# Optimization experiments

Hardware: AMD Instinct MI355X
Metric: run time of the kernel (lower is better)

Reference implementation:

```python
import jax, jax.numpy as jnp
import numpy as np

D_MODEL = 1024
HEAD_DIM = D_MODEL // 16  # num_heads=16, used only for the softmax scale
EPS = 1e-5


def _layernorm(x, g, b):
    mu = jnp.mean(x, axis=-1, keepdims=True)
    var = jnp.var(x, axis=-1, keepdims=True)
    return (x - mu) * jax.lax.rsqrt(var + EPS) * g + b


def setup_inputs() -> dict:
    key = jax.random.key(0)
    ks = jax.random.split(key, 16)
    d, dff = D_MODEL, 4 * D_MODEL
    s = 1.0 / np.sqrt(d)
    inp = {
        "x": jax.random.normal(ks[0], (4, 2048, d), dtype=jnp.float32),
        "wq": jax.random.normal(ks[1], (d, d), dtype=jnp.float32) * s,
        "bq": jnp.zeros((d,), jnp.float32),
        "wk": jax.random.normal(ks[2], (d, d), dtype=jnp.float32) * s,
        "bk": jnp.zeros((d,), jnp.float32),
        "wv": jax.random.normal(ks[3], (d, d), dtype=jnp.float32) * s,
        "bv": jnp.zeros((d,), jnp.float32),
        "wo": jax.random.normal(ks[4], (d, d), dtype=jnp.float32) * s,
        "bo": jnp.zeros((d,), jnp.float32),
        "w1": jax.random.normal(ks[5], (d, dff), dtype=jnp.float32) * s,
        "b1": jnp.zeros((dff,), jnp.float32),
        "w2": jax.random.normal(ks[6], (dff, d), dtype=jnp.float32) * (1.0 / np.sqrt(dff)),
        "b2": jnp.zeros((d,), jnp.float32),
        "g1": jnp.ones((d,), jnp.float32),
        "be1": jnp.zeros((d,), jnp.float32),
        "g2": jnp.ones((d,), jnp.float32),
        "be2": jnp.zeros((d,), jnp.float32),
    }
    return inp


def reference(x, wq, bq, wk, bk, wv, bv, wo, bo, w1, b1, w2, b2, g1, be1, g2, be2):
    # --- attention sub-block (NOTE: no head split in original module) ---
    residual = x
    h = _layernorm(x, g1, be1)
    q = h @ wq + bq
    k = h @ wk + bk
    v = h @ wv + bv
    scale = 1.0 / np.sqrt(HEAD_DIM)
    scores = jnp.einsum("bsd,btd->bst", q, k) * scale  # [B,S,S]
    attn = jax.nn.softmax(scores, axis=-1)
    ctx = jnp.einsum("bst,btd->bsd", attn, v)
    x = ctx @ wo + bo + residual
    # --- MLP sub-block ---
    residual = x
    h = _layernorm(x, g2, be2)
    h = jax.nn.gelu(h @ w1 + b1, approximate=False)
    return h @ w2 + b2 + residual
```

## Files before the change

kernel.cpp:

```cpp
#include <hip/hip_runtime.h>
#include <hip/hip_bf16.h>

typedef __hip_bfloat16 bf16;
typedef __attribute__((ext_vector_type(8))) short short8;
typedef __attribute__((ext_vector_type(4))) float floatx4;
typedef __attribute__((address_space(3))) char c3;

template <int V> struct ic { static constexpr int value = V; };

__device__ __forceinline__ unsigned short f2bf(float x) {
  unsigned u = __builtin_bit_cast(unsigned, x);
  unsigned r = (u + 0x7fffu + ((u >> 16) & 1u)) >> 16;
  return (unsigned short)r;
}

#define GLL(g, l) __builtin_amdgcn_global_load_lds(                                  \
    (const __attribute__((address_space(1))) void*)(g),                              \
    (__attribute__((address_space(3))) void*)(l), 16, 0, 0)

template <int N> __device__ __forceinline__ void vmwait() {
  asm volatile("s_waitcnt vmcnt(%0)" ::"i"(N) : "memory");
}
template <int OFF> __device__ __forceinline__ short8 dsr(unsigned a) {
  short8 r;
  asm volatile("ds_read_b128 %0, %1 offset:%2" : "=v"(r) : "v"(a), "i"(OFF));
  return r;
}
__device__ __forceinline__ void lgkm0_fence() {
  asm volatile("s_waitcnt lgkmcnt(0)" ::: "memory");
  __builtin_amdgcn_sched_barrier(0);
}

__global__ __launch_bounds__(256) void wtrans_kernel(const float* __restrict__ in,
                                                     bf16* __restrict__ out,
                                                     int K, int N) {
  __shared__ float tile[32][33];
  int tx = threadIdx.x, ty = threadIdx.y;
  int n0 = blockIdx.x * 32, k0 = blockIdx.y * 32;
#pragma unroll
  for (int i = 0; i < 32; i += 8)
    tile[ty + i][tx] = in[(size_t)(k0 + ty + i) * N + (n0 + tx)];
  __syncthreads();
#pragma unroll
  for (int i = 0; i < 32; i += 8)
    out[(size_t)(n0 + ty + i) * K + (k0 + tx)] = __float2bfloat16(tile[tx][ty + i]);
}

__global__ __launch_bounds__(256) void ln_kernel(const float* __restrict__ x,
                                                 const float* __restrict__ g,
                                                 const float* __restrict__ b,
                                                 bf16* __restrict__ out) {
  const int D = 1024;
  size_t row = blockIdx.x;
  int t = threadIdx.x;
  float4 v = ((const float4*)(x + row * D))[t];
  float s  = v.x + v.y + v.z + v.w;
  float ss = v.x * v.x + v.y * v.y + v.z * v.z + v.w * v.w;
#pragma unroll
  for (int off = 32; off > 0; off >>= 1) {
    s  += __shfl_xor(s, off);
    ss += __shfl_xor(ss, off);
  }
  __shared__ float rs[4], rss[4];
  int wv = t >> 6;
  if ((t & 63) == 0) { rs[wv] = s; rss[wv] = ss; }
  __syncthreads();
  s  = rs[0] + rs[1] + rs[2] + rs[3];
  ss = rss[0] + rss[1] + rss[2] + rss[3];
  float mu  = s * (1.f / D);
  float inv = rsqrtf(ss * (1.f / D) - mu * mu + 1e-5f);
  float4 gv = ((const float4*)g)[t];
  float4 bv = ((const float4*)b)[t];
  ushort4 o;
  o.x = f2bf((v.x - mu) * inv * gv.x + bv.x);
  o.y = f2bf((v.y - mu) * inv * gv.y + bv.y);
  o.z = f2bf((v.z - mu) * inv * gv.z + bv.z);
  o.w = f2bf((v.w - mu) * inv * gv.w + bv.w);
  ((ushort4*)(out + row * D))[t] = o;
}

__global__ __launch_bounds__(256) void softmax_kernel(float* sc) {
  const int S = 2048;
  float* p = sc + (size_t)blockIdx.x * S;
  int t = threadIdx.x;
  float4 v0 = ((const float4*)p)[2 * t];
  float4 v1 = ((const float4*)p)[2 * t + 1];
  float f[8] = {v0.x, v0.y, v0.z, v0.w, v1.x, v1.y, v1.z, v1.w};
  float m = f[0];
#pragma unroll
  for (int j = 1; j < 8; ++j) m = fmaxf(m, f[j]);
#pragma unroll
  for (int off = 32; off > 0; off >>= 1) m = fmaxf(m, __shfl_xor(m, off));
  __shared__ float r1[4], r2[4];
  int wv = t >> 6;
  if ((t & 63) == 0) r1[wv] = m;
  __syncthreads();
  m = fmaxf(fmaxf(r1[0], r1[1]), fmaxf(r1[2], r1[3]));
  float s = 0.f;
#pragma unroll
  for (int j = 0; j < 8; ++j) { f[j] = __expf(f[j] - m); s += f[j]; }
#pragma unroll
  for (int off = 32; off > 0; off >>= 1) s += __shfl_xor(s, off);
  if ((t & 63) == 0) r2[wv] = s;
  __syncthreads();
  s = r2[0] + r2[1] + r2[2] + r2[3];
  float inv = 1.f / s;
  unsigned u0 = f2bf(f[0] * inv), u1 = f2bf(f[1] * inv);
  unsigned u2 = f2bf(f[2] * inv), u3 = f2bf(f[3] * inv);
  unsigned u4 = f2bf(f[4] * inv), u5 = f2bf(f[5] * inv);
  unsigned u6 = f2bf(f[6] * inv), u7 = f2bf(f[7] * inv);
  uint4 o;
  o.x = u0 | (u1 << 16);
  o.y = u2 | (u3 << 16);
  o.z = u4 | (u5 << 16);
  o.w = u6 | (u7 << 16);
  ((uint4*)p)[t] = o;
}

template <int NF, bool OUT_BF16, bool HAS_BIAS, bool HAS_RES, bool GELU, bool VTR>
__global__ __launch_bounds__(512, 2) void gemm7(
    const bf16* __restrict__ A, int lda, size_t sA,
    const bf16* __restrict__ BT, int ldb, size_t sB,
    void* Cv, size_t sC,
    const float* __restrict__ bias, const float* res, bf16* vtr,
    int N, int K, float alpha, int gx, int gy) {
  constexpr int BN = NF * 64;
  constexpr int NI = NF / 2;
  constexpr int BHALF = NF == 4 ? 16384 : 8192;
  __shared__ __align__(16) char lds_storage[65536 + (NF == 4 ? 65536 : 32768)];
  const unsigned ldsAu = (unsigned)(uintptr_t)(c3*)lds_storage;
  const unsigned ldsBu = ldsAu + 65536;

  const int tid = threadIdx.x;
  const int lane = tid & 63;
  const int wave = tid >> 6;
  const int wm = wave >> 2, wn = wave & 3;
  const int lr = lane & 15, lq = lane >> 4;

  int id = blockIdx.x;
  const int nwg = gridDim.x;
  if ((nwg & 7) == 0) id = (id & 7) * (nwg >> 3) + (id >> 3);
  const int bx = id % gx;
  const int rem = id / gx;
  const int by = rem % gy;
  const int bz = rem / gy;
  const int m0 = by * 256, n0 = bx * BN;

  const int srow = tid >> 3;
  const int schunk = ((tid & 7) ^ (srow & 7)) * 8;
  const bf16* gA = A + sA * bz + (size_t)(m0 + srow) * lda + schunk;
  const bf16* gB = BT + sB * bz + (size_t)(n0 + srow) * ldb + schunk;

  const int nk = K >> 6;

  auto stA = [&](int tt, int h) {
    const bf16* s = gA + (size_t)(h * 128) * lda + (size_t)tt * 64;
    char* d = lds_storage + (((tt & 1) * 2 + h) << 14) + tid * 16;
    GLL(s, d);
    GLL(s + (size_t)64 * lda, d + 8192);
  };
  auto stB = [&](int tt, int h) {
    const bf16* s = gB + (size_t)(h * (BN / 2)) * ldb + (size_t)tt * 64;
    char* d = lds_storage + 65536 + ((tt & 1) * 2 + h) * BHALF + tid * 16;
    GLL(s, d);
    if constexpr (NF == 4) GLL(s + (size_t)64 * ldb, d + 8192);
  };

  const unsigned aB0 = (wm * 64 + lr) * 128 + ((lq ^ (lr & 7)) << 4);
  const unsigned bRow = (NF == 4) ? (wn * 32 + lr) : (wn * 16 + lr);
  const unsigned bB0 = bRow * 128 + ((lq ^ (lr & 7)) << 4);

  floatx4 acc[2][2][4][NI] = {};

  stA(0, 0); stB(0, 0); stB(0, 1); stA(0, 1);
  stA(1, 0); stB(1, 0); stB(1, 1);
  vmwait<NF == 4 ? 10 : 7>();
  __builtin_amdgcn_s_barrier();

  auto tile_body = [&](int t, auto modeC) {
    constexpr int MODE = decltype(modeC)::value;
    constexpr int W0  = MODE < 2 ? (NF == 4 ? 10 : 8) : 2;
    constexpr int W1  = MODE == 0 ? (NF == 4 ? 12 : 9)
                                  : (MODE == 1 ? (NF == 4 ? 8 : 6) : 0);
    constexpr int W23 = MODE == 0 ? (NF == 4 ? 10 : 7)
                                  : (MODE == 1 ? (NF == 4 ? 4 : 3) : -1);
    const unsigned As0 = ldsAu + (((t & 1) * 2 + 0) << 14);
    const unsigned As1 = As0 + 16384;
    const unsigned Bs0 = ldsBu + ((t & 1) * 2 + 0) * BHALF;
    const unsigned Bs1 = Bs0 + BHALF;
    short8 a0[4], a1[4], b0[NI], b1[NI], bb0[NI], bb1[NI];

    {
      const unsigned aA = As0 + aB0, aX = aA ^ 64;
      a0[0] = dsr<0>(aA);  a0[1] = dsr<2048>(aA);  a0[2] = dsr<4096>(aA);  a0[3] = dsr<6144>(aA);
      a1[0] = dsr<0>(aX);  a1[1] = dsr<2048>(aX);  a1[2] = dsr<4096>(aX);  a1[3] = dsr<6144>(aX);
      const unsigned bA = Bs0 + bB0, bX = bA ^ 64;
      bb0[0] = dsr<0>(bA); bb1[0] = dsr<0>(bX);
      if constexpr (NI > 1) { bb0[1] = dsr<2048>(bA); bb1[1] = dsr<2048>(bX); }
    }
    if constexpr (MODE < 2) stA(t + 1, 1);
    lgkm0_fence();
    __builtin_amdgcn_s_setprio(1);
#pragma unroll
    for (int mi = 0; mi < 4; ++mi)
#pragma unroll
      for (int ni = 0; ni < NI; ++ni)
        acc[0][0][mi][ni] = __builtin_amdgcn_mfma_f32_16x16x32_bf16(a0[mi], bb0[ni], acc[0][0][mi][ni], 0, 0, 0);
#pragma unroll
    for (int mi = 0; mi < 4; ++mi)
#pragma unroll
      for (int ni = 0; ni < NI; ++ni)
        acc[0][0][mi][ni] = __builtin_amdgcn_mfma_f32_16x16x32_bf16(a1[mi], bb1[ni], acc[0][0][mi][ni], 0, 0, 0);
    __builtin_amdgcn_s_setprio(0);
    vmwait<W0>();
    __builtin_amdgcn_s_barrier();

    {
      const unsigned bA = Bs1 + bB0, bX = bA ^ 64;
      b0[0] = dsr<0>(bA); b1[0] = dsr<0>(bX);
      if constexpr (NI > 1) { b0[1] = dsr<2048>(bA); b1[1] = dsr<2048>(bX); }
    }
    if constexpr (MODE == 0) { stA(t + 2, 0); stB(t + 2, 0); }
    lgkm0_fence();
    __builtin_amdgcn_s_setprio(1);
#pragma unroll
    for (int mi = 0; mi < 4; ++mi)
#pragma unroll
      for (int ni = 0; ni < NI; ++ni)
        acc[0][1][mi][ni] = __builtin_amdgcn_mfma_f32_16x16x32_bf16(a0[mi], b0[ni], acc[0][1][mi][ni], 0, 0, 0);
#pragma unroll
    for (int mi = 0; mi < 4; ++mi)
#pragma unroll
      for (int ni = 0; ni < NI; ++ni)
        acc[0][1][mi][ni] = __builtin_amdgcn_mfma_f32_16x16x32_bf16(a1[mi], b1[ni], acc[0][1][mi][ni], 0, 0, 0);
    __builtin_amdgcn_s_setprio(0);
    vmwait<W1>();
    __builtin_amdgcn_s_barrier();

    {
      const unsigned aA = As1 + aB0, aX = aA ^ 64;
      a0[0] = dsr<0>(aA);  a0[1] = dsr<2048>(aA);  a0[2] = dsr<4096>(aA);  a0[3] = dsr<6144>(aA);
      a1[0] = dsr<0>(aX);  a1[1] = dsr<2048>(aX);  a1[2] = dsr<4096>(aX);  a1[3] = dsr<6144>(aX);
    }
    if constexpr (MODE == 0) stB(t + 2, 1);
    lgkm0_fence();
    __builtin_amdgcn_s_setprio(1);
#pragma unroll
    for (int mi = 0; mi < 4; ++mi)
#pragma unroll
      for (int ni = 0; ni < NI; ++ni)
        acc[1][1][mi][ni] = __builtin_amdgcn_mfma_f32_16x16x32_bf16(a0[mi], b0[ni], acc[1][1][mi][ni], 0, 0, 0);
#pragma unroll
    for (int mi = 0; mi < 4; ++mi)
#pragma unroll
      for (int ni = 0; ni < NI; ++ni)
        acc[1][1][mi][ni] = __builtin_amdgcn_mfma_f32_16x16x32_bf16(a1[mi], b1[ni], acc[1][1][mi][ni], 0, 0, 0);
#pragma unroll
    for (int mi = 0; mi < 4; ++mi)
#pragma unroll
      for (int ni = 0; ni < NI; ++ni)
        acc[1][0][mi][ni] = __builtin_amdgcn_mfma_f32_16x16x32_bf16(a0[mi], bb0[ni], acc[1][0][mi][ni], 0, 0, 0);
#pragma unroll
    for (int mi = 0; mi < 4; ++mi)
#pragma unroll
      for (int ni = 0; ni < NI; ++ni)
        acc[1][0][mi][ni] = __builtin_amdgcn_mfma_f32_16x16x32_bf16(a1[mi], bb1[ni], acc[1][0][mi][ni], 0, 0, 0);
    __builtin_amdgcn_s_setprio(0);
    if constexpr (W23 >= 0) {
      vmwait<W23>();
      __builtin_amdgcn_s_barrier();
    }
  };

  for (int t = 0; t + 2 < nk; ++t) tile_body(t, ic<0>{});
  tile_body(nk - 2, ic<1>{});
  tile_body(nk - 1, ic<2>{});

  float* Cf = (float*)Cv;
  bf16* Cb = (bf16*)Cv;
  const size_t cb = sC * bz;
#pragma unroll
  for (int mq = 0; mq < 2; ++mq)
#pragma unroll
    for (int nq = 0; nq < 2; ++nq)
#pragma unroll
      for (int mi = 0; mi < 4; ++mi) {
        const int row = m0 + mq * 128 + wm * 64 + mi * 16 + lq * 4;
#pragma unroll
        for (int ni = 0; ni < NI; ++ni) {
          const int col = n0 + nq * (BN / 2) + wn * (BN / 8) + ni * 16 + lr;
          const float bb = HAS_BIAS ? bias[col] : 0.f;
#pragma unroll
          for (int r = 0; r < 4; ++r) {
            float val = acc[mq][nq][mi][ni][r] * alpha + bb;
            if (GELU) val = 0.5f * val * (1.f + erff(val * 0.70710678118654752f));
            if (HAS_RES) val += res[(size_t)(row + r) * N + col];
            const size_t idx = cb + (size_t)(row + r) * N + col;
            if (OUT_BF16) Cb[idx] = __float2bfloat16(val);
            else Cf[idx] = val;
            if (VTR) {
              if (col >= 2048) {
                const int rr = row + r;
                vtr[(((size_t)(rr >> 11) << 10) + (col - 2048)) * 2048 + (rr & 2047)] =
                    __float2bfloat16(val);
              }
            }
          }
        }
      }
}

extern "C" void kernel_launch(void* const* d_in, const int* in_sizes, int n_in,
                              void* d_out, int out_size, void* d_ws, size_t ws_size,
                              hipStream_t stream) {
  const int B = 4, S = 2048, D = 1024, DFF = 4096;
  const int M = B * S;
  const float* x   = (const float*)d_in[0];
  const float* wq  = (const float*)d_in[1];
  const float* bq  = (const float*)d_in[2];
  const float* wk  = (const float*)d_in[3];
  const float* bk  = (const float*)d_in[4];
  const float* wv  = (const float*)d_in[5];
  const float* bv  = (const float*)d_in[6];
  const float* wo  = (const float*)d_in[7];
  const float* bo  = (const float*)d_in[8];
  const float* w1  = (const float*)d_in[9];
  const float* b1  = (const float*)d_in[10];
  const float* w2  = (const float*)d_in[11];
  const float* b2  = (const float*)d_in[12];
  const float* g1  = (const float*)d_in[13];
  const float* be1 = (const float*)d_in[14];
  const float* g2  = (const float*)d_in[15];
  const float* be2 = (const float*)d_in[16];
  float* out = (float*)d_out;

  char* wsb = (char*)d_ws;
  const size_t MB1 = 1ull << 20;
  bf16* wqkvT = (bf16*)(wsb + 0 * MB1);
  bf16* woT   = (bf16*)(wsb + 6 * MB1);
  bf16* w1T   = (bf16*)(wsb + 8 * MB1);
  bf16* w2T   = (bf16*)(wsb + 16 * MB1);
  float* bqkv = (float*)(wsb + 24 * MB1);
  bf16* h     = (bf16*)(wsb + 25 * MB1);
  bf16* qkv   = (bf16*)(wsb + 41 * MB1);
  bf16* hidden = (bf16*)(wsb + 41 * MB1);
  bf16* vTall = (bf16*)(wsb + 89 * MB1);
  float* sc   = (float*)(wsb + 105 * MB1);

  int chunk = 1;
  if (ws_size > 105 * MB1) {
    size_t c = (ws_size - 105 * MB1) / (16 * MB1);
    chunk = (int)(c > 4 ? 4 : (c < 1 ? 1 : c));
  }

  dim3 tb(32, 8);
  wtrans_kernel<<<dim3(32, 32), tb, 0, stream>>>(wq, wqkvT, D, D);
  wtrans_kernel<<<dim3(32, 32), tb, 0, stream>>>(wk, wqkvT + (size_t)1024 * 1024, D, D);
  wtrans_kernel<<<dim3(32, 32), tb, 0, stream>>>(wv, wqkvT + (size_t)2048 * 1024, D, D);
  wtrans_kernel<<<dim3(32, 32), tb, 0, stream>>>(wo, woT, D, D);
  wtrans_kernel<<<dim3(128, 32), tb, 0, stream>>>(w1, w1T, D, DFF);
  wtrans_kernel<<<dim3(32, 128), tb, 0, stream>>>(w2, w2T, DFF, D);
  hipMemcpyAsync(bqkv, bq, 4096, hipMemcpyDeviceToDevice, stream);
  hipMemcpyAsync(bqkv + 1024, bk, 4096, hipMemcpyDeviceToDevice, stream);
  hipMemcpyAsync(bqkv + 2048, bv, 4096, hipMemcpyDeviceToDevice, stream);

  ln_kernel<<<M, 256, 0, stream>>>(x, g1, be1, h);

  gemm7<2, true, true, false, false, true><<<24 * 32, 512, 0, stream>>>(
      h, D, 0, wqkvT, D, 0, qkv, 0, bqkv, nullptr, vTall, 3072, D, 1.f, 24, 32);

  for (int b0 = 0; b0 < B; b0 += chunk) {
    int c = (B - b0 < chunk) ? (B - b0) : chunk;
    gemm7<4, false, false, false, false, false><<<64 * c, 512, 0, stream>>>(
        qkv + (size_t)b0 * S * 3072, 3072, (size_t)S * 3072,
        qkv + (size_t)b0 * S * 3072 + 1024, 3072, (size_t)S * 3072,
        sc, (size_t)S * S, nullptr, nullptr, nullptr, S, D, 0.125f, 8, 8);
    softmax_kernel<<<c * S, 256, 0, stream>>>(sc);
    gemm7<2, true, false, false, false, false><<<64 * c, 512, 0, stream>>>(
        (const bf16*)sc, 2 * S, (size_t)S * 2 * S,
        vTall + (size_t)b0 * D * S, S, (size_t)D * S,
        h + (size_t)b0 * S * D, (size_t)S * D, nullptr, nullptr, nullptr, D, S, 1.f, 8, 8);
  }

  gemm7<2, false, true, true, false, false><<<8 * 32, 512, 0, stream>>>(
      h, D, 0, woT, D, 0, out, 0, bo, x, nullptr, D, D, 1.f, 8, 32);

  ln_kernel<<<M, 256, 0, stream>>>(out, g2, be2, h);

  gemm7<4, true, true, false, true, false><<<16 * 32, 512, 0, stream>>>(
      h, D, 0, w1T, D, 0, hidden, 0, b1, nullptr, nullptr, DFF, D, 1.f, 16, 32);

  gemm7<2, false, true, true, false, false><<<8 * 32, 512, 0, stream>>>(
      hidden, DFF, 0, w2T, DFF, 0, out, 0, b2, out, nullptr, D, DFF, 1.f, 8, 32);
}
```

Baseline: 459.2 us.

## Rewrite GEMM main loop with cross-tile register prefetch and drop 256-wide tile variant

```diff
diff --git a/kernel.cpp b/kernel.cpp
--- a/kernel.cpp
+++ b/kernel.cpp
@@ -21,15 +21,16 @@
 template <int N> __device__ __forceinline__ void vmwait() {
   asm volatile("s_waitcnt vmcnt(%0)" ::"i"(N) : "memory");
 }
+template <int N> __device__ __forceinline__ void lgkwait() {
+  asm volatile("s_waitcnt lgkmcnt(%0)" ::"i"(N) : "memory");
+  __builtin_amdgcn_sched_barrier(0);
+}
 template <int OFF> __device__ __forceinline__ short8 dsr(unsigned a) {
   short8 r;
   asm volatile("ds_read_b128 %0, %1 offset:%2" : "=v"(r) : "v"(a), "i"(OFF));
   return r;
 }
-__device__ __forceinline__ void lgkm0_fence() {
-  asm volatile("s_waitcnt lgkmcnt(0)" ::: "memory");
-  __builtin_amdgcn_sched_barrier(0);
-}
+#define MFMA_(d, a, b) d = __builtin_amdgcn_mfma_f32_16x16x32_bf16(a, b, d, 0, 0, 0)
 
 __global__ __launch_bounds__(256) void wtrans_kernel(const float* __restrict__ in,
                                                      bf16* __restrict__ out,
@@ -117,17 +118,14 @@
   ((uint4*)p)[t] = o;
 }
 
-template <int NF, bool OUT_BF16, bool HAS_BIAS, bool HAS_RES, bool GELU, bool VTR>
-__global__ __launch_bounds__(512, 2) void gemm7(
+template <bool OUT_BF16, bool HAS_BIAS, bool HAS_RES, bool GELU, bool VTR>
+__global__ __launch_bounds__(512, 2) void gemm8(
     const bf16* __restrict__ A, int lda, size_t sA,
     const bf16* __restrict__ BT, int ldb, size_t sB,
     void* Cv, size_t sC,
     const float* __restrict__ bias, const float* res, bf16* vtr,
     int N, int K, float alpha, int gx, int gy) {
-  constexpr int BN = NF * 64;
-  constexpr int NI = NF / 2;
-  constexpr int BHALF = NF == 4 ? 16384 : 8192;
-  __shared__ __align__(16) char lds_storage[65536 + (NF == 4 ? 65536 : 32768)];
+  __shared__ __align__(16) char lds_storage[65536 + 32768];
   const unsigned ldsAu = (unsigned)(uintptr_t)(c3*)lds_storage;
   const unsigned ldsBu = ldsAu + 65536;
 
@@ -144,7 +142,7 @@
   const int rem = id / gx;
   const int by = rem % gy;
   const int bz = rem / gy;
-  const int m0 = by * 256, n0 = bx * BN;
+  const int m0 = by * 256, n0 = bx * 128;
 
   const int srow = tid >> 3;
   const int schunk = ((tid & 7) ^ (srow & 7)) * 8;
@@ -160,121 +158,102 @@
     GLL(s + (size_t)64 * lda, d + 8192);
   };
   auto stB = [&](int tt, int h) {
-    const bf16* s = gB + (size_t)(h * (BN / 2)) * ldb + (size_t)tt * 64;
-    char* d = lds_storage + 65536 + ((tt & 1) * 2 + h) * BHALF + tid * 16;
+    const bf16* s = gB + (size_t)(h * 64) * ldb + (size_t)tt * 64;
+    char* d = lds_storage + 65536 + ((tt & 1) * 2 + h) * 8192 + tid * 16;
     GLL(s, d);
-    if constexpr (NF == 4) GLL(s + (size_t)64 * ldb, d + 8192);
   };
 
   const unsigned aB0 = (wm * 64 + lr) * 128 + ((lq ^ (lr & 7)) << 4);
-  const unsigned bRow = (NF == 4) ? (wn * 32 + lr) : (wn * 16 + lr);
-  const unsigned bB0 = bRow * 128 + ((lq ^ (lr & 7)) << 4);
-
-  floatx4 acc[2][2][4][NI] = {};
+  const unsigned bB0 = (wn * 16 + lr) * 128 + ((lq ^ (lr & 7)) << 4);
+
+  floatx4 acc[2][2][4] = {};
+  short8 am0k0[4], am0k1[4];
+  short8 bn0Ak0, bn0Ak1, bn0Bk0, bn0Bk1;
 
   stA(0, 0); stB(0, 0); stB(0, 1); stA(0, 1);
-  stA(1, 0); stB(1, 0); stB(1, 1);
-  vmwait<NF == 4 ? 10 : 7>();
+  stA(1, 0); stB(1, 0); stB(1, 1); stA(1, 1);
+  vmwait<8>();
   __builtin_amdgcn_s_barrier();
-
-  auto tile_body = [&](int t, auto modeC) {
+  {
+    const unsigned aA = ldsAu + aB0, aX = aA ^ 64;
+    am0k0[0] = dsr<0>(aA); am0k0[1] = dsr<2048>(aA); am0k0[2] = dsr<4096>(aA); am0k0[3] = dsr<6144>(aA);
+    am0k1[0] = dsr<0>(aX); am0k1[1] = dsr<2048>(aX); am0k1[2] = dsr<4096>(aX); am0k1[3] = dsr<6144>(aX);
+    const unsigned bA = ldsBu + bB0;
+    bn0Ak0 = dsr<0>(bA); bn0Ak1 = dsr<0>(bA ^ 64);
+  }
+
+  auto body = [&](int t, auto modeC, short8& bu0, short8& bu1, short8& bw0, short8& bw1) {
     constexpr int MODE = decltype(modeC)::value;
-    constexpr int W0  = MODE < 2 ? (NF == 4 ? 10 : 8) : 2;
-    constexpr int W1  = MODE == 0 ? (NF == 4 ? 12 : 9)
-                                  : (MODE == 1 ? (NF == 4 ? 8 : 6) : 0);
-    constexpr int W23 = MODE == 0 ? (NF == 4 ? 10 : 7)
-                                  : (MODE == 1 ? (NF == 4 ? 4 : 3) : -1);
-    const unsigned As0 = ldsAu + (((t & 1) * 2 + 0) << 14);
-    const unsigned As1 = As0 + 16384;
-    const unsigned Bs0 = ldsBu + ((t & 1) * 2 + 0) * BHALF;
-    const unsigned Bs1 = Bs0 + BHALF;
-    short8 a0[4], a1[4], b0[NI], b1[NI], bb0[NI], bb1[NI];
-
+    const unsigned As1 = ldsAu + ((((unsigned)t & 1) * 2 + 1) << 14);
+    const unsigned Bs1 = ldsBu + (((unsigned)t & 1) * 2 + 1) * 8192;
+
+    short8 bn1k0, bn1k1;
     {
-      const unsigned aA = As0 + aB0, aX = aA ^ 64;
-      a0[0] = dsr<0>(aA);  a0[1] = dsr<2048>(aA);  a0[2] = dsr<4096>(aA);  a0[3] = dsr<6144>(aA);
-      a1[0] = dsr<0>(aX);  a1[1] = dsr<2048>(aX);  a1[2] = dsr<4096>(aX);  a1[3] = dsr<6144>(aX);
-      const unsigned bA = Bs0 + bB0, bX = bA ^ 64;
-      bb0[0] = dsr<0>(bA); bb1[0] = dsr<0>(bX);
-      if constexpr (NI > 1) { bb0[1] = dsr<2048>(bA); bb1[1] = dsr<2048>(bX); }
+      const unsigned bA = Bs1 + bB0;
+      bn1k0 = dsr<0>(bA); bn1k1 = dsr<0>(bA ^ 64);
     }
-    if constexpr (MODE < 2) stA(t + 1, 1);
-    lgkm0_fence();
+    lgkwait<2>();
     __builtin_amdgcn_s_setprio(1);
 #pragma unroll
-    for (int mi = 0; mi < 4; ++mi)
-#pragma unroll
-      for (int ni = 0; ni < NI; ++ni)
-        acc[0][0][mi][ni] = __builtin_amdgcn_mfma_f32_16x16x32_bf16(a0[mi], bb0[ni], acc[0][0][mi][ni], 0, 0, 0);
-#pragma unroll
-    for (int mi = 0; mi < 4; ++mi)
-#pragma unroll
-      for (int ni = 0; ni < NI; ++ni)
-        acc[0][0][mi][ni] = __builtin_amdgcn_mfma_f32_16x16x32_bf16(a1[mi], bb1[ni], acc[0][0][mi][ni], 0, 0, 0);
+    for (int mi = 0; mi < 4; ++mi) MFMA_(acc[0][0][mi], am0k0[mi], bu0);
+#pragma unroll
+    for (int mi = 0; mi < 4; ++mi) MFMA_(acc[0][0][mi], am0k1[mi], bu1);
     __builtin_amdgcn_s_setprio(0);
-    vmwait<W0>();
+    vmwait<MODE == 2 ? 0 : 6>();
     __builtin_amdgcn_s_barrier();
 
+    short8 am1k0[4], am1k1[4];
     {
-      const unsigned bA = Bs1 + bB0, bX = bA ^ 64;
-      b0[0] = dsr<0>(bA); b1[0] = dsr<0>(bX);
-      if constexpr (NI > 1) { b0[1] = dsr<2048>(bA); b1[1] = dsr<2048>(bX); }
+      const unsigned aA = As1 + aB0, aX = aA ^ 64;
+      am1k0[0] = dsr<0>(aA); am1k0[1] = dsr<2048>(aA); am1k0[2] = dsr<4096>(aA); am1k0[3] = dsr<6144>(aA);
+      am1k1[0] = dsr<0>(aX); am1k1[1] = dsr<2048>(aX); am1k1[2] = dsr<4096>(aX); am1k1[3] = dsr<6144>(aX);
     }
     if constexpr (MODE == 0) { stA(t + 2, 0); stB(t + 2, 0); }
-    lgkm0_fence();
+    lgkwait<8>();
     __builtin_amdgcn_s_setprio(1);
 #pragma unroll
-    for (int mi = 0; mi < 4; ++mi)
-#pragma unroll
-      for (int ni = 0; ni < NI; ++ni)
-        acc[0][1][mi][ni] = __builtin_amdgcn_mfma_f32_16x16x32_bf16(a0[mi], b0[ni], acc[0][1][mi][ni], 0, 0, 0);
-#pragma unroll
-    for (int mi = 0; mi < 4; ++mi)
-#pragma unroll
-      for (int ni = 0; ni < NI; ++ni)
-        acc[0][1][mi][ni] = __builtin_amdgcn_mfma_f32_16x16x32_bf16(a1[mi], b1[ni], acc[0][1][mi][ni], 0, 0, 0);
+    for (int mi = 0; mi < 4; ++mi) MFMA_(acc[0][1][mi], am0k0[mi], bn1k0);
+#pragma unroll
+    for (int mi = 0; mi < 4; ++mi) MFMA_(acc[0][1][mi], am0k1[mi], bn1k1);
     __builtin_amdgcn_s_setprio(0);
-    vmwait<W1>();
-    __builtin_amdgcn_s_barrier();
-
-    {
-      const unsigned aA = As1 + aB0, aX = aA ^ 64;
-      a0[0] = dsr<0>(aA);  a0[1] = dsr<2048>(aA);  a0[2] = dsr<4096>(aA);  a0[3] = dsr<6144>(aA);
-      a1[0] = dsr<0>(aX);  a1[1] = dsr<2048>(aX);  a1[2] = dsr<4096>(aX);  a1[3] = dsr<6144>(aX);
+    if constexpr (MODE == 0) { vmwait<6>(); __builtin_amdgcn_s_barrier(); }
+    else if constexpr (MODE == 1) { vmwait<3>(); __builtin_amdgcn_s_barrier(); }
+
+    if constexpr (MODE < 2) {
+      const unsigned aA = ldsAu + ((((unsigned)(t + 1) & 1) * 2) << 14) + aB0, aX = aA ^ 64;
+      am0k0[0] = dsr<0>(aA); am0k0[1] = dsr<2048>(aA); am0k0[2] = dsr<4096>(aA); am0k0[3] = dsr<6144>(aA);
+      am0k1[0] = dsr<0>(aX); am0k1[1] = dsr<2048>(aX); am0k1[2] = dsr<4096>(aX); am0k1[3] = dsr<6144>(aX);
+      const unsigned bA = ldsBu + (((unsigned)(t + 1) & 1) * 2) * 8192 + bB0;
+      bw0 = dsr<0>(bA); bw1 = dsr<0>(bA ^ 64);
     }
     if constexpr (MODE == 0) stB(t + 2, 1);
-    lgkm0_fence();
+    if constexpr (MODE < 2) lgkwait<10>();
+    else lgkwait<0>();
     __builtin_amdgcn_s_setprio(1);
 #pragma unroll
-    for (int mi = 0; mi < 4; ++mi)
-#pragma unroll
-      for (int ni = 0; ni < NI; ++ni)
-        acc[1][1][mi][ni] = __builtin_amdgcn_mfma_f32_16x16x32_bf16(a0[mi], b0[ni], acc[1][1][mi][ni], 0, 0, 0);
-#pragma unroll
-    for (int mi = 0; mi < 4; ++mi)
-#pragma unroll
-      for (int ni = 0; ni < NI; ++ni)
-        acc[1][1][mi][ni] = __builtin_amdgcn_mfma_f32_16x16x32_bf16(a1[mi], b1[ni], acc[1][1][mi][ni], 0, 0, 0);
-#pragma unroll
-    for (int mi = 0; mi < 4; ++mi)
-#pragma unroll
-      for (int ni = 0; ni < NI; ++ni)
-        acc[1][0][mi][ni] = __builtin_amdgcn_mfma_f32_16x16x32_bf16(a0[mi], bb0[ni], acc[1][0][mi][ni], 0, 0, 0);
-#pragma unroll
-    for (int mi = 0; mi < 4; ++mi)
-#pragma unroll
-      for (int ni = 0; ni < NI; ++ni)
-        acc[1][0][mi][ni] = __builtin_amdgcn_mfma_f32_16x16x32_bf16(a1[mi], bb1[ni], acc[1][0][mi][ni], 0, 0, 0);
+    for (int mi = 0; mi < 4; ++mi) MFMA_(acc[1][1][mi], am1k0[mi], bn1k0);
+#pragma unroll
+    for (int mi = 0; mi < 4; ++mi) MFMA_(acc[1][1][mi], am1k1[mi], bn1k1);
     __builtin_amdgcn_s_setprio(0);
-    if constexpr (W23 >= 0) {
-      vmwait<W23>();
-      __builtin_amdgcn_s_barrier();
-    }
+    if constexpr (MODE < 2) __builtin_amdgcn_s_barrier();
+
+    if constexpr (MODE == 0) stA(t + 2, 1);
+    __builtin_amdgcn_s_setprio(1);
+#pragma unroll
+    for (int mi = 0; mi < 4; ++mi) MFMA_(acc[1][0][mi], am1k0[mi], bu0);
+#pragma unroll
+    for (int mi = 0; mi < 4; ++mi) MFMA_(acc[1][0][mi], am1k1[mi], bu1);
+    __builtin_amdgcn_s_setprio(0);
+    if constexpr (MODE == 0) { vmwait<8>(); __builtin_amdgcn_s_barrier(); }
+    else if constexpr (MODE == 1) { vmwait<2>(); __builtin_amdgcn_s_barrier(); }
   };
 
-  for (int t = 0; t + 2 < nk; ++t) tile_body(t, ic<0>{});
-  tile_body(nk - 2, ic<1>{});
-  tile_body(nk - 1, ic<2>{});
+  for (int t = 0; t + 2 < nk; t += 2) {
+    body(t, ic<0>{}, bn0Ak0, bn0Ak1, bn0Bk0, bn0Bk1);
+    body(t + 1, ic<0>{}, bn0Bk0, bn0Bk1, bn0Ak0, bn0Ak1);
+  }
+  body(nk - 2, ic<1>{}, bn0Ak0, bn0Ak1, bn0Bk0, bn0Bk1);
+  body(nk - 1, ic<2>{}, bn0Bk0, bn0Bk1, bn0Ak0, bn0Ak1);
 
   float* Cf = (float*)Cv;
   bf16* Cb = (bf16*)Cv;
@@ -286,24 +265,21 @@
 #pragma unroll
       for (int mi = 0; mi < 4; ++mi) {
         const int row = m0 + mq * 128 + wm * 64 + mi * 16 + lq * 4;
-#pragma unroll
-        for (int ni = 0; ni < NI; ++ni) {
-          const int col = n0 + nq * (BN / 2) + wn * (BN / 8) + ni * 16 + lr;
-          const float bb = HAS_BIAS ? bias[col] : 0.f;
-#pragma unroll
-          for (int r = 0; r < 4; ++r) {
-            float val = acc[mq][nq][mi][ni][r] * alpha + bb;
-            if (GELU) val = 0.5f * val * (1.f + erff(val * 0.70710678118654752f));
-            if (HAS_RES) val += res[(size_t)(row + r) * N + col];
-            const size_t idx = cb + (size_t)(row + r) * N + col;
-            if (OUT_BF16) Cb[idx] = __float2bfloat16(val);
-            else Cf[idx] = val;
-            if (VTR) {
-              if (col >= 2048) {
-                const int rr = row + r;
-                vtr[(((size_t)(rr >> 11) << 10) + (col - 2048)) * 2048 + (rr & 2047)] =
-                    __float2bfloat16(val);
-              }
+        const int col = n0 + nq * 64 + wn * 16 + lr;
+        const float bb = HAS_BIAS ? bias[col] : 0.f;
+#pragma unroll
+        for (int r = 0; r < 4; ++r) {
+          float val = acc[mq][nq][mi][r] * alpha + bb;
+          if (GELU) val = 0.5f * val * (1.f + erff(val * 0.70710678118654752f));
+          if (HAS_RES) val += res[(size_t)(row + r) * N + col];
+          const size_t idx = cb + (size_t)(row + r) * N + col;
+          if (OUT_BF16) Cb[idx] = __float2bfloat16(val);
+          else Cf[idx] = val;
+          if (VTR) {
+            if (col >= 2048) {
+              const int rr = row + r;
+              vtr[(((size_t)(rr >> 11) << 10) + (col - 2048)) * 2048 + (rr & 2047)] =
+                  __float2bfloat16(val);
             }
           }
         }
@@ -366,30 +342,30 @@
 
   ln_kernel<<<M, 256, 0, stream>>>(x, g1, be1, h);
 
-  gemm7<2, true, true, false, false, true><<<24 * 32, 512, 0, stream>>>(
+  gemm8<true, true, false, false, true><<<24 * 32, 512, 0, stream>>>(
       h, D, 0, wqkvT, D, 0, qkv, 0, bqkv, nullptr, vTall, 3072, D, 1.f, 24, 32);
 
   for (int b0 = 0; b0 < B; b0 += chunk) {
     int c = (B - b0 < chunk) ? (B - b0) : chunk;
-    gemm7<4, false, false, false, false, false><<<64 * c, 512, 0, stream>>>(
+    gemm8<false, false, false, false, false><<<128 * c, 512, 0, stream>>>(
         qkv + (size_t)b0 * S * 3072, 3072, (size_t)S * 3072,
         qkv + (size_t)b0 * S * 3072 + 1024, 3072, (size_t)S * 3072,
-        sc, (size_t)S * S, nullptr, nullptr, nullptr, S, D, 0.125f, 8, 8);
+        sc, (size_t)S * S, nullptr, nullptr, nullptr, S, D, 0.125f, 16, 8);
     softmax_kernel<<<c * S, 256, 0, stream>>>(sc);
-    gemm7<2, true, false, false, false, false><<<64 * c, 512, 0, stream>>>(
+    gemm8<true, false, false, false, false><<<64 * c, 512, 0, stream>>>(
         (const bf16*)sc, 2 * S, (size_t)S * 2 * S,
         vTall + (size_t)b0 * D * S, S, (size_t)D * S,
         h + (size_t)b0 * S * D, (size_t)S * D, nullptr, nullptr, nullptr, D, S, 1.f, 8, 8);
   }
 
-  gemm7<2, false, true, true, false, false><<<8 * 32, 512, 0, stream>>>(
+  gemm8<false, true, true, false, false><<<8 * 32, 512, 0, stream>>>(
       h, D, 0, woT, D, 0, out, 0, bo, x, nullptr, D, D, 1.f, 8, 32);
 
   ln_kernel<<<M, 256, 0, stream>>>(out, g2, be2, h);
 
-  gemm7<4, true, true, false, true, false><<<16 * 32, 512, 0, stream>>>(
-      h, D, 0, w1T, D, 0, hidden, 0, b1, nullptr, nullptr, DFF, D, 1.f, 16, 32);
-
-  gemm7<2, false, true, true, false, false><<<8 * 32, 512, 0, stream>>>(
+  gemm8<true, true, false, true, false><<<32 * 32, 512, 0, stream>>>(
+      h, D, 0, w1T, D, 0, hidden, 0, b1, nullptr, nullptr, DFF, D, 1.f, 32, 32);
+
+  gemm8<false, true, true, false, false><<<8 * 32, 512, 0, stream>>>(
       hidden, DFF, 0, w2T, DFF, 0, out, 0, b2, out, nullptr, D, DFF, 1.f, 8, 32);
 }
```

New measurement: 463.9 us. Within noise of the previous version (+1.0%).

## Merge weight transposes into one launch and run softmax one wave per row

Applied to the files above, without the earlier changes.

```diff
diff --git a/kernel.cpp b/kernel.cpp
--- a/kernel.cpp
+++ b/kernel.cpp
@@ -31,12 +31,46 @@
   __builtin_amdgcn_sched_barrier(0);
 }
 
-__global__ __launch_bounds__(256) void wtrans_kernel(const float* __restrict__ in,
-                                                     bf16* __restrict__ out,
-                                                     int K, int N) {
+__global__ __launch_bounds__(256) void wtrans_all(
+    const float* __restrict__ wq, const float* __restrict__ wk,
+    const float* __restrict__ wv, const float* __restrict__ wo,
+    const float* __restrict__ w1, const float* __restrict__ w2,
+    bf16* __restrict__ wqkvT, bf16* __restrict__ woT,
+    bf16* __restrict__ w1T, bf16* __restrict__ w2T,
+    const float* __restrict__ bq, const float* __restrict__ bk,
+    const float* __restrict__ bv, float* __restrict__ bqkv) {
+  const int id = blockIdx.x;
+  if (id == 12288) {
+    int t = threadIdx.y * 32 + threadIdx.x;
+    for (int i = t; i < 1024; i += 256) {
+      bqkv[i] = bq[i];
+      bqkv[1024 + i] = bk[i];
+      bqkv[2048 + i] = bv[i];
+    }
+    return;
+  }
+  const float* in;
+  bf16* out;
+  int K, N, bx, by;
+  if (id < 4096) {
+    const int seg = id >> 10, r = id & 1023;
+    bx = r & 31; by = r >> 5; K = 1024; N = 1024;
+    if (seg == 0) { in = wq; out = wqkvT; }
+    else if (seg == 1) { in = wk; out = wqkvT + (size_t)1024 * 1024; }
+    else if (seg == 2) { in = wv; out = wqkvT + (size_t)2048 * 1024; }
+    else { in = wo; out = woT; }
+  } else if (id < 8192) {
+    const int r = id - 4096;
+    bx = r & 127; by = r >> 7; K = 1024; N = 4096;
+    in = w1; out = w1T;
+  } else {
+    const int r = id - 8192;
+    bx = r & 31; by = r >> 5; K = 4096; N = 1024;
+    in = w2; out = w2T;
+  }
   __shared__ float tile[32][33];
-  int tx = threadIdx.x, ty = threadIdx.y;
-  int n0 = blockIdx.x * 32, k0 = blockIdx.y * 32;
+  const int tx = threadIdx.x, ty = threadIdx.y;
+  const int n0 = bx * 32, k0 = by * 32;
 #pragma unroll
   for (int i = 0; i < 32; i += 8)
     tile[ty + i][tx] = in[(size_t)(k0 + ty + i) * N + (n0 + tx)];
@@ -79,42 +113,35 @@
   ((ushort4*)(out + row * D))[t] = o;
 }
 
-__global__ __launch_bounds__(256) void softmax_kernel(float* sc) {
+__global__ __launch_bounds__(256) void softmax_wave(float* sc) {
   const int S = 2048;
-  float* p = sc + (size_t)blockIdx.x * S;
-  int t = threadIdx.x;
-  float4 v0 = ((const float4*)p)[2 * t];
-  float4 v1 = ((const float4*)p)[2 * t + 1];
-  float f[8] = {v0.x, v0.y, v0.z, v0.w, v1.x, v1.y, v1.z, v1.w};
+  const int wave = threadIdx.x >> 6, lane = threadIdx.x & 63;
+  float* p = sc + ((size_t)blockIdx.x * 4 + wave) * S;
+  float f[32];
+  const float4* pv = (const float4*)p;
+#pragma unroll
+  for (int j = 0; j < 8; ++j) {
+    float4 v = pv[lane + 64 * j];
+    f[4 * j] = v.x; f[4 * j + 1] = v.y; f[4 * j + 2] = v.z; f[4 * j + 3] = v.w;
+  }
   float m = f[0];
 #pragma unroll
-  for (int j = 1; j < 8; ++j) m = fmaxf(m, f[j]);
+  for (int j = 1; j < 32; ++j) m = fmaxf(m, f[j]);
 #pragma unroll
   for (int off = 32; off > 0; off >>= 1) m = fmaxf(m, __shfl_xor(m, off));
-  __shared__ float r1[4], r2[4];
-  int wv = t >> 6;
-  if ((t & 63) == 0) r1[wv] = m;
-  __syncthreads();
-  m = fmaxf(fmaxf(r1[0], r1[1]), fmaxf(r1[2], r1[3]));
   float s = 0.f;
 #pragma unroll
-  for (int j = 0; j < 8; ++j) { f[j] = __expf(f[j] - m); s += f[j]; }
+  for (int j = 0; j < 32; ++j) { f[j] = __expf(f[j] - m); s += f[j]; }
 #pragma unroll
   for (int off = 32; off > 0; off >>= 1) s += __shfl_xor(s, off);
-  if ((t & 63) == 0) r2[wv] = s;
-  __syncthreads();
-  s = r2[0] + r2[1] + r2[2] + r2[3];
-  float inv = 1.f / s;
-  unsigned u0 = f2bf(f[0] * inv), u1 = f2bf(f[1] * inv);
-  unsigned u2 = f2bf(f[2] * inv), u3 = f2bf(f[3] * inv);
-  unsigned u4 = f2bf(f[4] * inv), u5 = f2bf(f[5] * inv);
-  unsigned u6 = f2bf(f[6] * inv), u7 = f2bf(f[7] * inv);
-  uint4 o;
-  o.x = u0 | (u1 << 16);
-  o.y = u2 | (u3 << 16);
-  o.z = u4 | (u5 << 16);
-  o.w = u6 | (u7 << 16);
-  ((uint4*)p)[t] = o;
+  const float inv = 1.f / s;
+  uint2* po = (uint2*)p;
+#pragma unroll
+  for (int j = 0; j < 8; ++j) {
+    unsigned lo = (unsigned)f2bf(f[4 * j] * inv) | ((unsigned)f2bf(f[4 * j + 1] * inv) << 16);
+    unsigned hi = (unsigned)f2bf(f[4 * j + 2] * inv) | ((unsigned)f2bf(f[4 * j + 3] * inv) << 16);
+    po[lane + 64 * j] = make_uint2(lo, hi);
+  }
 }
 
 template <int NF, bool OUT_BF16, bool HAS_BIAS, bool HAS_RES, bool GELU, bool VTR>
@@ -215,10 +242,11 @@
     vmwait<W0>();
     __builtin_amdgcn_s_barrier();
 
+    short8 b0l[NI], b1l[NI];
     {
       const unsigned bA = Bs1 + bB0, bX = bA ^ 64;
-      b0[0] = dsr<0>(bA); b1[0] = dsr<0>(bX);
-      if constexpr (NI > 1) { b0[1] = dsr<2048>(bA); b1[1] = dsr<2048>(bX); }
+      b0l[0] = dsr<0>(bA); b1l[0] = dsr<0>(bX);
+      if constexpr (NI > 1) { b0l[1] = dsr<2048>(bA); b1l[1] = dsr<2048>(bX); }
     }
     if constexpr (MODE == 0) { stA(t + 2, 0); stB(t + 2, 0); }
     lgkm0_fence();
@@ -227,12 +255,12 @@
     for (int mi = 0; mi < 4; ++mi)
 #pragma unroll
       for (int ni = 0; ni < NI; ++ni)
-        acc[0][1][mi][ni] = __builtin_amdgcn_mfma_f32_16x16x32_bf16(a0[mi], b0[ni], acc[0][1][mi][ni], 0, 0, 0);
-#pragma unroll
-    for (int mi = 0; mi < 4; ++mi)
-#pragma unroll
-      for (int ni = 0; ni < NI; ++ni)
-        acc[0][1][mi][ni] = __builtin_amdgcn_mfma_f32_16x16x32_bf16(a1[mi], b1[ni], acc[0][1][mi][ni], 0, 0, 0);
+        acc[0][1][mi][ni] = __builtin_amdgcn_mfma_f32_16x16x32_bf16(a0[mi], b0l[ni], acc[0][1][mi][ni], 0, 0, 0);
+#pragma unroll
+    for (int mi = 0; mi < 4; ++mi)
+#pragma unroll
+      for (int ni = 0; ni < NI; ++ni)
+        acc[0][1][mi][ni] = __builtin_amdgcn_mfma_f32_16x16x32_bf16(a1[mi], b1l[ni], acc[0][1][mi][ni], 0, 0, 0);
     __builtin_amdgcn_s_setprio(0);
     vmwait<W1>();
     __builtin_amdgcn_s_barrier();
@@ -249,12 +277,12 @@
     for (int mi = 0; mi < 4; ++mi)
 #pragma unroll
       for (int ni = 0; ni < NI; ++ni)
-        acc[1][1][mi][ni] = __builtin_amdgcn_mfma_f32_16x16x32_bf16(a0[mi], b0[ni], acc[1][1][mi][ni], 0, 0, 0);
-#pragma unroll
-    for (int mi = 0; mi < 4; ++mi)
-#pragma unroll
-      for (int ni = 0; ni < NI; ++ni)
-        acc[1][1][mi][ni] = __builtin_amdgcn_mfma_f32_16x16x32_bf16(a1[mi], b1[ni], acc[1][1][mi][ni], 0, 0, 0);
+        acc[1][1][mi][ni] = __builtin_amdgcn_mfma_f32_16x16x32_bf16(a0[mi], b0l[ni], acc[1][1][mi][ni], 0, 0, 0);
+#pragma unroll
+    for (int mi = 0; mi < 4; ++mi)
+#pragma unroll
+      for (int ni = 0; ni < NI; ++ni)
+        acc[1][1][mi][ni] = __builtin_amdgcn_mfma_f32_16x16x32_bf16(a1[mi], b1l[ni], acc[1][1][mi][ni], 0, 0, 0);
 #pragma unroll
     for (int mi = 0; mi < 4; ++mi)
 #pragma unroll
@@ -353,16 +381,8 @@
     chunk = (int)(c > 4 ? 4 : (c < 1 ? 1 : c));
   }
 
-  dim3 tb(32, 8);
-  wtrans_kernel<<<dim3(32, 32), tb, 0, stream>>>(wq, wqkvT, D, D);
-  wtrans_kernel<<<dim3(32, 32), tb, 0, stream>>>(wk, wqkvT + (size_t)1024 * 1024, D, D);
-  wtrans_kernel<<<dim3(32, 32), tb, 0, stream>>>(wv, wqkvT + (size_t)2048 * 1024, D, D);
-  wtrans_kernel<<<dim3(32, 32), tb, 0, stream>>>(wo, woT, D, D);
-  wtrans_kernel<<<dim3(128, 32), tb, 0, stream>>>(w1, w1T, D, DFF);
-  wtrans_kernel<<<dim3(32, 128), tb, 0, stream>>>(w2, w2T, DFF, D);
-  hipMemcpyAsync(bqkv, bq, 4096, hipMemcpyDeviceToDevice, stream);
-  hipMemcpyAsync(bqkv + 1024, bk, 4096, hipMemcpyDeviceToDevice, stream);
-  hipMemcpyAsync(bqkv + 2048, bv, 4096, hipMemcpyDeviceToDevice, stream);
+  wtrans_all<<<12289, dim3(32, 8), 0, stream>>>(
+      wq, wk, wv, wo, w1, w2, wqkvT, woT, w1T, w2T, bq, bk, bv, bqkv);
 
   ln_kernel<<<M, 256, 0, stream>>>(x, g1, be1, h);
 
@@ -375,7 +395,7 @@
         qkv + (size_t)b0 * S * 3072, 3072, (size_t)S * 3072,
         qkv + (size_t)b0 * S * 3072 + 1024, 3072, (size_t)S * 3072,
         sc, (size_t)S * S, nullptr, nullptr, nullptr, S, D, 0.125f, 8, 8);
-    softmax_kernel<<<c * S, 256, 0, stream>>>(sc);
+    softmax_wave<<<c * S / 4, 256, 0, stream>>>(sc);
     gemm7<2, true, false, false, false, false><<<64 * c, 512, 0, stream>>>(
         (const bf16*)sc, 2 * S, (size_t)S * 2 * S,
         vTall + (size_t)b0 * D * S, S, (size_t)D * S,
```

Result: faster. 443.5 us (-3.4%).
